# Optimization experiments

Measured on AMD Instinct MI355X. Metric: run time of the kernel, lower is better.

Reference implementation:

```python
import jax, jax.numpy as jnp
import numpy as np

N_NODES = 100000
N_EDGES = 1000000
N_INPUT = 64
N_HIDDEN = 64
K = 8


def setup_inputs() -> dict:
    key = jax.random.key(0)
    k1, k2, k3, k4 = jax.random.split(key, 4)
    x = jax.random.normal(k1, (N_NODES, N_INPUT), dtype=jnp.float32)
    edge_index = jax.random.randint(k2, (2, N_EDGES), 0, N_NODES, dtype=jnp.int64)
    # ChebConv has K independent [in, out] weight matrices (Glorot-ish scale) and a bias.
    weight = jax.random.normal(k3, (K, N_INPUT, N_HIDDEN), dtype=jnp.float32) * (1.0 / np.sqrt(N_INPUT))
    bias = jax.random.normal(k4, (N_HIDDEN,), dtype=jnp.float32) * 0.01
    return {"x": x, "edge_index": edge_index, "weight": weight, "bias": bias}


def _cheb_edge_norm(edge_index, num_nodes):
    # PyG ChebConv sym normalization with default lambda_max=2.0:
    #   L_hat = (2/lambda_max) * (I - D^-1/2 A D^-1/2) - I = -D^-1/2 A D^-1/2
    # (the diagonal +1 from the Laplacian and the -1 self-loop cancel exactly).
    src, dst = edge_index[0], edge_index[1]
    ones = jnp.ones(src.shape[0], dtype=jnp.float32)
    deg = jax.ops.segment_sum(ones, src, num_segments=num_nodes)
    deg_inv_sqrt = jnp.where(deg > 0, jax.lax.rsqrt(jnp.maximum(deg, 1.0)), 0.0)
    return -deg_inv_sqrt[src] * deg_inv_sqrt[dst]  # [E]


def reference(x, edge_index, weight, bias):
    num_nodes = x.shape[0]
    src, dst = edge_index[0], edge_index[1]
    norm = _cheb_edge_norm(edge_index, num_nodes)

    def prop(h):  # h: [N, F] -> L_hat @ h via gather-multiply-scatter over edges
        return jax.ops.segment_sum(norm[:, None] * h[src], dst, num_segments=num_nodes)

    # Chebyshev recursion: T0 = x, T1 = L_hat x, Tk = 2 L_hat T_{k-1} - T_{k-2}
    Tx0 = x
    out = Tx0 @ weight[0]
    Tx1 = prop(Tx0)
    out = out + Tx1 @ weight[1]
    for k in range(2, weight.shape[0]):
        Tx2 = 2.0 * prop(Tx1) - Tx0
        out = out + Tx2 @ weight[k]
        Tx0, Tx1 = Tx1, Tx2
    out = out + bias
    # bn=False path: ReLU then dropout (identity in eval mode)
    return jax.nn.relu(out)
```

## Files before the change

### kernel.cpp

```cpp
#include <hip/hip_runtime.h>
#include <hip/hip_bf16.h>

typedef __attribute__((ext_vector_type(8))) short s16x8;
typedef __attribute__((ext_vector_type(4))) float f32x4;

#define HC 48
#define RBH 6400
#define RBS 3200

static __device__ __forceinline__ unsigned short f2bf(float f) {
    unsigned int u = __float_as_uint(f);
    unsigned int r = (u + 0x7FFFu + ((u >> 16) & 1u)) >> 16;
    return (unsigned short)r;
}

__global__ __launch_bounds__(256) void k_hist(const int* __restrict__ eidx,
                                              unsigned short* __restrict__ partials,
                                              int N, int E, int HR) {
    __shared__ int h[RBH];
    int b = blockIdx.x;
    int job = b / (HR * HC);
    int rc = b % (HR * HC);
    int r = rc / HC, c = rc % HC;
    int lo = r * RBH;
    int nb = min(RBH, N - lo);
    if (nb <= 0) return;
    for (int i = threadIdx.x; i < nb; i += 256) h[i] = 0;
    __syncthreads();
    const int* vals = eidx + (size_t)job * E;
    int e0 = (int)(((long long)E * c / HC) & ~3LL);
    int e1 = (c == HC - 1) ? E : (int)(((long long)E * (c + 1) / HC) & ~3LL);
    int e = e0 + threadIdx.x * 4;
    for (; e + 4 <= e1; e += 1024) {
        int4 v = *reinterpret_cast<const int4*>(vals + e);
        unsigned r0 = (unsigned)(v.x - lo), r1 = (unsigned)(v.y - lo);
        unsigned r2 = (unsigned)(v.z - lo), r3 = (unsigned)(v.w - lo);
        if (r0 < (unsigned)nb) atomicAdd(&h[r0], 1);
        if (r1 < (unsigned)nb) atomicAdd(&h[r1], 1);
        if (r2 < (unsigned)nb) atomicAdd(&h[r2], 1);
        if (r3 < (unsigned)nb) atomicAdd(&h[r3], 1);
    }
    if (threadIdx.x == 0)
        for (int t = e1 & ~3; t < e1; ++t) {
            unsigned rel = (unsigned)(vals[t] - lo);
            if (rel < (unsigned)nb) atomicAdd(&h[rel], 1);
        }
    __syncthreads();
    unsigned short* outp = partials + ((size_t)(job * HC + c)) * N + lo;
    for (int i = threadIdx.x; i < nb; i += 256) outp[i] = (unsigned short)h[i];
}

__global__ void k_reduce(const unsigned short* __restrict__ partials,
                         float* __restrict__ dis, int* __restrict__ cnt, int N) {
    int n = blockIdx.x * blockDim.x + threadIdx.x;
    if (n >= N) return;
    int dsum = 0, csum = 0;
    for (int c = 0; c < HC; ++c) {
        dsum += partials[(size_t)c * N + n];
        csum += partials[(size_t)(HC + c) * N + n];
    }
    dis[n] = dsum > 0 ? rsqrtf((float)dsum) : 0.f;
    cnt[n] = csum;
}

__global__ void k_scan1(const int* __restrict__ cnt, int* __restrict__ incl,
                        int* __restrict__ bsum, int N) {
    __shared__ int sm[1024];
    int t = threadIdx.x;
    int i = blockIdx.x * 1024 + t;
    sm[t] = (i < N) ? cnt[i] : 0;
    __syncthreads();
    for (int off = 1; off < 1024; off <<= 1) {
        int add = (t >= off) ? sm[t - off] : 0;
        __syncthreads();
        sm[t] += add;
        __syncthreads();
    }
    if (i < N) incl[i] = sm[t];
    if (t == 1023) bsum[blockIdx.x] = sm[1023];
}

__global__ void k_scan2(const int* __restrict__ bsum, int* __restrict__ boff,
                        int nb, int* __restrict__ rowptr, int N) {
    if (threadIdx.x == 0 && blockIdx.x == 0) {
        int run = 0;
        for (int b = 0; b < nb; ++b) { boff[b] = run; run += bsum[b]; }
        rowptr[N] = run;
    }
}

__global__ void k_scan3(const int* __restrict__ cnt, const int* __restrict__ boff,
                        int* __restrict__ rowptr,
                        const unsigned short* __restrict__ pdst,
                        int* __restrict__ cbase, int N) {
    int i = blockIdx.x * 1024 + threadIdx.x;
    if (i >= N) return;
    int ex = rowptr[i] - cnt[i] + boff[blockIdx.x];
    rowptr[i] = ex;
    int run = ex;
    for (int c = 0; c < HC; ++c) {
        size_t idx = (size_t)c * N + i;
        cbase[idx] = run;
        run += pdst[idx];
    }
}

__global__ __launch_bounds__(256) void k_scatter(
        const int* __restrict__ src, const int* __restrict__ dst,
        const int* __restrict__ cbase, int* __restrict__ srcs, int N, int E) {
    __shared__ int cur[RBS];
    int r = blockIdx.x / HC, c = blockIdx.x % HC;
    int lo = r * RBS;
    int nb = min(RBS, N - lo);
    if (nb <= 0) return;
    for (int i = threadIdx.x; i < nb; i += 256)
        cur[i] = cbase[(size_t)c * N + lo + i];
    __syncthreads();
    int e0 = (int)(((long long)E * c / HC) & ~3LL);
    int e1 = (c == HC - 1) ? E : (int)(((long long)E * (c + 1) / HC) & ~3LL);
    int e = e0 + threadIdx.x * 4;
    for (; e + 4 <= e1; e += 1024) {
        int4 d4 = *reinterpret_cast<const int4*>(dst + e);
        unsigned r0 = (unsigned)(d4.x - lo), r1 = (unsigned)(d4.y - lo);
        unsigned r2 = (unsigned)(d4.z - lo), r3 = (unsigned)(d4.w - lo);
        if (r0 < (unsigned)nb) srcs[atomicAdd(&cur[r0], 1)] = src[e];
        if (r1 < (unsigned)nb) srcs[atomicAdd(&cur[r1], 1)] = src[e + 1];
        if (r2 < (unsigned)nb) srcs[atomicAdd(&cur[r2], 1)] = src[e + 2];
        if (r3 < (unsigned)nb) srcs[atomicAdd(&cur[r3], 1)] = src[e + 3];
    }
    if (threadIdx.x == 0)
        for (int t = e1 & ~3; t < e1; ++t) {
            unsigned rel = (unsigned)(dst[t] - lo);
            if (rel < (unsigned)nb) srcs[atomicAdd(&cur[rel], 1)] = src[t];
        }
}

__global__ void k_pack(const float* __restrict__ x, const float* __restrict__ dis,
                       const float* __restrict__ W,
                       unsigned short* __restrict__ tb0, unsigned short* __restrict__ ysA,
                       unsigned short* __restrict__ ysB, unsigned short* __restrict__ wt,
                       int N, int K) {
    int t = blockIdx.x * blockDim.x + threadIdx.x;
    int nys = (N + 1) * 32;
    if (t < nys) {
        int row = t >> 5, p = t & 31;
        size_t o = ((size_t)row << 6) + (p << 1);
        if (row == N) {
            *(unsigned*)(ysA + o) = 0;
            *(unsigned*)(ysB + o) = 0;
            return;
        }
        float2 v = *reinterpret_cast<const float2*>(x + o);
        float dv = dis[row];
        *(unsigned*)(tb0 + o) = (unsigned)f2bf(v.x) | ((unsigned)f2bf(v.y) << 16);
        *(unsigned*)(ysA + o) = (unsigned)f2bf(v.x * dv) | ((unsigned)f2bf(v.y * dv) << 16);
    } else {
        int u = t - nys;
        if (u < K * 4096) {
            float v = W[u];
            int k = u >> 12;
            int r = u & 4095;
            int i = r >> 6;
            int j = r & 63;
            wt[(size_t)j * (K * 64) + (k << 6) + i] = f2bf(v);
        }
    }
}

static __device__ __forceinline__ void addrow(float* acc, uint4 t) {
    acc[0] += __uint_as_float(t.x << 16);
    acc[1] += __uint_as_float(t.x & 0xffff0000u);
    acc[2] += __uint_as_float(t.y << 16);
    acc[3] += __uint_as_float(t.y & 0xffff0000u);
    acc[4] += __uint_as_float(t.z << 16);
    acc[5] += __uint_as_float(t.z & 0xffff0000u);
    acc[6] += __uint_as_float(t.w << 16);
    acc[7] += __uint_as_float(t.w & 0xffff0000u);
}

__global__ __launch_bounds__(256) void k_prop(
        const unsigned short* __restrict__ Ysin,
        const unsigned short* __restrict__ Tm2,
        unsigned short* __restrict__ Tout,
        unsigned short* __restrict__ Ysout,
        const int* __restrict__ rowptr, const int* __restrict__ srcs,
        const float* __restrict__ dis,
        int N, int E, float scale, float beta, int wys) {
    int gt = blockIdx.x * blockDim.x + threadIdx.x;
    int wave0 = (gt >> 6) << 3;
    int lane = gt & 63;
    int g = lane >> 3;
    int i = lane & 7;
    int node = wave0 + g;
    bool live = node < N;
    int rs = 0, deg = 0;
    if (live) {
        rs = rowptr[node];
        deg = rowptr[node + 1] - rs;
    }
    int wmax = deg;
#pragma unroll
    for (int m = 8; m <= 32; m <<= 1) {
        int o = __shfl_xor(wmax, m);
        wmax = o > wmax ? o : wmax;
    }
    float acc[8];
#pragma unroll
    for (int j = 0; j < 8; ++j) acc[j] = 0.f;
    for (int e = 0; e < wmax; e += 8) {
        int b = rs + e;
        int s[8];
#pragma unroll
        for (int q = 0; q < 8; ++q)
            s[q] = (e + q < deg) ? srcs[min(b + q, E - 1)] : N;
        uint4 t[8];
#pragma unroll
        for (int q = 0; q < 8; ++q)
            t[q] = *reinterpret_cast<const uint4*>(Ysin + ((size_t)s[q] << 6) + (i << 3));
#pragma unroll
        for (int q = 0; q < 8; ++q) addrow(acc, t[q]);
    }
    if (live) {
        float dv = dis[node];
        float sc = -scale * dv;
        size_t base = ((size_t)node << 6) + (i << 3);
        float r[8];
#pragma unroll
        for (int j = 0; j < 8; ++j) r[j] = sc * acc[j];
        if (beta != 0.f) {
            uint4 pv = *reinterpret_cast<const uint4*>(Tm2 + base);
            r[0] = fmaf(beta, __uint_as_float(pv.x << 16), r[0]);
            r[1] = fmaf(beta, __uint_as_float(pv.x & 0xffff0000u), r[1]);
            r[2] = fmaf(beta, __uint_as_float(pv.y << 16), r[2]);
            r[3] = fmaf(beta, __uint_as_float(pv.y & 0xffff0000u), r[3]);
            r[4] = fmaf(beta, __uint_as_float(pv.z << 16), r[4]);
            r[5] = fmaf(beta, __uint_as_float(pv.z & 0xffff0000u), r[5]);
            r[6] = fmaf(beta, __uint_as_float(pv.w << 16), r[6]);
            r[7] = fmaf(beta, __uint_as_float(pv.w & 0xffff0000u), r[7]);
        }
        uint4 ov;
        ov.x = (unsigned)f2bf(r[0]) | ((unsigned)f2bf(r[1]) << 16);
        ov.y = (unsigned)f2bf(r[2]) | ((unsigned)f2bf(r[3]) << 16);
        ov.z = (unsigned)f2bf(r[4]) | ((unsigned)f2bf(r[5]) << 16);
        ov.w = (unsigned)f2bf(r[6]) | ((unsigned)f2bf(r[7]) << 16);
        *reinterpret_cast<uint4*>(Tout + base) = ov;
        if (wys) {
            uint4 yv;
            yv.x = (unsigned)f2bf(r[0] * dv) | ((unsigned)f2bf(r[1] * dv) << 16);
            yv.y = (unsigned)f2bf(r[2] * dv) | ((unsigned)f2bf(r[3] * dv) << 16);
            yv.z = (unsigned)f2bf(r[4] * dv) | ((unsigned)f2bf(r[5] * dv) << 16);
            yv.w = (unsigned)f2bf(r[6] * dv) | ((unsigned)f2bf(r[7] * dv) << 16);
            *reinterpret_cast<uint4*>(Ysout + base) = yv;
        }
    }
}

template <int KS>
__global__ __launch_bounds__(256) void k_gemm(const unsigned short* __restrict__ tb,
                                              const unsigned short* __restrict__ wt,
                                              const float* __restrict__ bias,
                                              float* __restrict__ out,
                                              int N, int NF) {
    constexpr int NB = KS / 2;
    __shared__ unsigned short lds[KS * 512];
    int lane = threadIdx.x & 63;
    int w = threadIdx.x >> 6;
    int l16 = lane & 15;
    int quad = lane >> 4;
    const int KI = KS * 32;

    s16x8 afr[KS];
    {
        const unsigned short* wrow = wt + (size_t)(w * 16 + l16) * KI + quad * 8;
#pragma unroll
        for (int ks = 0; ks < KS; ++ks)
            afr[ks] = *reinterpret_cast<const s16x8*>(wrow + ks * 32);
    }
    f32x4 bias4 = *reinterpret_cast<const f32x4*>(bias + w * 16 + quad * 4);

    int ntiles = N >> 4;
    for (int t = blockIdx.x; t < ntiles; t += gridDim.x) {
        const char* tilebase = (const char*)tb + (size_t)t * 2048;
#pragma unroll
        for (int inst = 0; inst < 2 * NB; ++inst) {
            if ((inst & 3) != w) continue;
            int kbuf = inst >> 1;
            int j = inst & 1;
            int p = j * 64 + lane;
            int nrow = p >> 3;
            int s = (p & 7) ^ (nrow & 7);
            const char* g = tilebase + (size_t)kbuf * NF * 2 + nrow * 128 + s * 16;
            __builtin_amdgcn_global_load_lds(
                (const __attribute__((address_space(1))) unsigned int*)g,
                (__attribute__((address_space(3))) unsigned int*)(lds + inst * 512),
                16, 0, 0);
        }
        __syncthreads();
        f32x4 acc = {0.f, 0.f, 0.f, 0.f};
#pragma unroll
        for (int ks = 0; ks < KS; ++ks) {
            int kbuf = ks >> 1, half = ks & 1;
            int sph = (half * 4 + quad) ^ (l16 & 7);
            s16x8 bf = *reinterpret_cast<const s16x8*>(
                lds + kbuf * 1024 + l16 * 64 + sph * 8);
            acc = __builtin_amdgcn_mfma_f32_16x16x32_bf16(afr[ks], bf, acc, 0, 0, 0);
        }
        float* orow = out + (size_t)(t * 16 + l16) * 64 + w * 16 + quad * 4;
        f32x4 r;
#pragma unroll
        for (int q = 0; q < 4; ++q) {
            float v = acc[q] + bias4[q];
            r[q] = v > 0.f ? v : 0.f;
        }
        *reinterpret_cast<f32x4*>(orow) = r;
        __syncthreads();
    }
}

extern "C" void kernel_launch(void* const* d_in, const int* in_sizes, int n_in,
                              void* d_out, int out_size, void* d_ws, size_t ws_size,
                              hipStream_t stream) {
    const float* x    = (const float*)d_in[0];
    const int*   eidx = (const int*)d_in[1];
    const float* W    = (const float*)d_in[2];
    const float* bias = (const float*)d_in[3];
    float* out = (float*)d_out;

    const int NF = in_sizes[0];
    const int N  = NF / 64;
    const int E  = in_sizes[1] / 2;
    const int K  = in_sizes[2] / 4096;

    const int* src = eidx;
    const int* dst = eidx + E;

    char* ws = (char*)d_ws;
    size_t off = 0;
    auto alloc = [&](size_t bytes) -> char* {
        char* p = ws + off;
        off = (off + bytes + 255) & ~(size_t)255;
        return p;
    };
    unsigned short* Tb = (unsigned short*)alloc((size_t)K * NF * 2);
    unsigned short* Ys[2];
    Ys[0] = (unsigned short*)alloc((size_t)(N + 1) * 64 * 2);
    Ys[1] = (unsigned short*)alloc((size_t)(N + 1) * 64 * 2);
    unsigned short* Wt = (unsigned short*)alloc((size_t)64 * K * 64 * 2);
    int*   srcs   = (int*)alloc((size_t)E * 4);
    int*   rowptr = (int*)alloc((size_t)(N + 1) * 4);
    int*   cnt    = (int*)alloc((size_t)N * 4);
    unsigned short* partials = (unsigned short*)alloc((size_t)2 * HC * N * 2);
    int*   cbase  = (int*)alloc((size_t)HC * N * 4);
    float* dis  = (float*)alloc((size_t)N * 4);
    int*   bsum = (int*)alloc(1024);
    int*   boff = (int*)alloc(1024);
    (void)ws_size; (void)n_in; (void)out_size;

    int HR = (N + RBH - 1) / RBH;
    int SR = (N + RBS - 1) / RBS;
    const unsigned short* pdst = partials + (size_t)HC * N;

    k_hist<<<2 * HR * HC, 256, 0, stream>>>(eidx, partials, N, E, HR);
    k_reduce<<<(N + 255) / 256, 256, 0, stream>>>(partials, dis, cnt, N);
    int nb = (N + 1023) / 1024;
    k_scan1<<<nb, 1024, 0, stream>>>(cnt, rowptr, bsum, N);
    k_scan2<<<1, 64, 0, stream>>>(bsum, boff, nb, rowptr, N);
    k_scan3<<<nb, 1024, 0, stream>>>(cnt, boff, rowptr, pdst, cbase, N);
    k_scatter<<<SR * HC, 256, 0, stream>>>(src, dst, cbase, srcs, N, E);
    int packn = (N + 1) * 32 + K * 4096;
    k_pack<<<(packn + 255) / 256, 256, 0, stream>>>(x, dis, W, Tb, Ys[0], Ys[1], Wt, N, K);

    int waves = (N + 7) / 8;
    int pblocks = (waves * 64 + 255) / 256;
    for (int p = 1; p < K; ++p) {
        float scale = (p == 1) ? 1.f : 2.f;
        float beta  = (p == 1) ? 0.f : -1.f;
        const unsigned short* Tm2 = Tb + (size_t)(p >= 2 ? p - 2 : 0) * NF;
        k_prop<<<pblocks, 256, 0, stream>>>(
            Ys[(p - 1) & 1], Tm2, Tb + (size_t)p * NF, Ys[p & 1],
            rowptr, srcs, dis, N, E, scale, beta, p < K - 1 ? 1 : 0);
    }

    if (K == 8)      k_gemm<16><<<1024, 256, 0, stream>>>(Tb, Wt, bias, out, N, NF);
    else if (K == 4) k_gemm<8><<<1024, 256, 0, stream>>>(Tb, Wt, bias, out, N, NF);
    else if (K == 2) k_gemm<4><<<1024, 256, 0, stream>>>(Tb, Wt, bias, out, N, NF);
    else if (K == 1) k_gemm<2><<<1024, 256, 0, stream>>>(Tb, Wt, bias, out, N, NF);
}
```

Before: 342.7 us.

## Sort nodes by degree and carry per-edge source weights in propagation

Result: slower. 507.4 us (+48.1%).

```diff
diff --git a/kernel.cpp b/kernel.cpp
--- a/kernel.cpp
+++ b/kernel.cpp
@@ -7,6 +7,7 @@
 #define HC 48
 #define RBH 6400
 #define RBS 3200
+#define DB 64
 
 static __device__ __forceinline__ unsigned short f2bf(float f) {
     unsigned int u = __float_as_uint(f);
@@ -135,27 +136,79 @@
         }
 }
 
-__global__ void k_pack(const float* __restrict__ x, const float* __restrict__ dis,
-                       const float* __restrict__ W,
-                       unsigned short* __restrict__ tb0, unsigned short* __restrict__ ysA,
-                       unsigned short* __restrict__ ysB, unsigned short* __restrict__ wt,
-                       int N, int K) {
+__global__ __launch_bounds__(256) void k_dhist(const int* __restrict__ cnt,
+                                               int* __restrict__ dpart, int N) {
+    __shared__ int h[DB];
+    if (threadIdx.x < DB) h[threadIdx.x] = 0;
+    __syncthreads();
+    int i = blockIdx.x * 256 + threadIdx.x;
+    if (i < N) atomicAdd(&h[min(cnt[i], DB - 1)], 1);
+    __syncthreads();
+    if (threadIdx.x < DB) dpart[blockIdx.x * DB + threadIdx.x] = h[threadIdx.x];
+}
+
+__global__ void k_dscan(int* __restrict__ dpart, int nb2) {
+    __shared__ int tot[DB], base[DB];
+    int b = threadIdx.x;
+    int run = 0;
+    for (int blk = 0; blk < nb2; ++blk) {
+        int v = dpart[blk * DB + b];
+        dpart[blk * DB + b] = run;
+        run += v;
+    }
+    tot[b] = run;
+    __syncthreads();
+    if (b == 0) {
+        int r = 0;
+        for (int j = 0; j < DB; ++j) { base[j] = r; r += tot[j]; }
+    }
+    __syncthreads();
+    for (int blk = 0; blk < nb2; ++blk)
+        dpart[blk * DB + b] += base[b];
+}
+
+__global__ __launch_bounds__(256) void k_dscat(const int* __restrict__ cnt,
+                                               const int* __restrict__ rowptr,
+                                               const int* __restrict__ dpart,
+                                               int* __restrict__ perm,
+                                               int2* __restrict__ rdeg, int N) {
+    __shared__ int cur[DB];
+    if (threadIdx.x < DB) cur[threadIdx.x] = dpart[blockIdx.x * DB + threadIdx.x];
+    __syncthreads();
+    int i = blockIdx.x * 256 + threadIdx.x;
+    if (i < N) {
+        int d = cnt[i];
+        int pos = atomicAdd(&cur[min(d, DB - 1)], 1);
+        perm[pos] = i;
+        rdeg[pos] = make_int2(rowptr[i], d);
+    }
+}
+
+__global__ void k_pay(const int* __restrict__ srcs, const float* __restrict__ dis,
+                      int2* __restrict__ pay, int E) {
+    int e = blockIdx.x * blockDim.x + threadIdx.x;
+    if (e < E) {
+        int s = srcs[e];
+        pay[e] = make_int2(s, __float_as_int(dis[s]));
+    }
+}
+
+__global__ void k_pack(const float* __restrict__ x, const float* __restrict__ W,
+                       unsigned short* __restrict__ tb, unsigned short* __restrict__ wt,
+                       int N, int K, int NR) {
     int t = blockIdx.x * blockDim.x + threadIdx.x;
-    int nys = (N + 1) * 32;
-    if (t < nys) {
+    int nx = N * 32;
+    if (t < nx) {
         int row = t >> 5, p = t & 31;
         size_t o = ((size_t)row << 6) + (p << 1);
-        if (row == N) {
-            *(unsigned*)(ysA + o) = 0;
-            *(unsigned*)(ysB + o) = 0;
-            return;
-        }
         float2 v = *reinterpret_cast<const float2*>(x + o);
-        float dv = dis[row];
-        *(unsigned*)(tb0 + o) = (unsigned)f2bf(v.x) | ((unsigned)f2bf(v.y) << 16);
-        *(unsigned*)(ysA + o) = (unsigned)f2bf(v.x * dv) | ((unsigned)f2bf(v.y * dv) << 16);
+        *(unsigned*)(tb + o) = (unsigned)f2bf(v.x) | ((unsigned)f2bf(v.y) << 16);
+    } else if (t < nx + K * 32) {
+        int u = t - nx;
+        int lvl = u >> 5, p = u & 31;
+        *(unsigned*)(tb + (size_t)lvl * NR + ((size_t)N << 6) + (p << 1)) = 0;
     } else {
-        int u = t - nys;
+        int u = t - nx - K * 32;
         if (u < K * 4096) {
             float v = W[u];
             int k = u >> 12;
@@ -167,36 +220,37 @@
     }
 }
 
-static __device__ __forceinline__ void addrow(float* acc, uint4 t) {
-    acc[0] += __uint_as_float(t.x << 16);
-    acc[1] += __uint_as_float(t.x & 0xffff0000u);
-    acc[2] += __uint_as_float(t.y << 16);
-    acc[3] += __uint_as_float(t.y & 0xffff0000u);
-    acc[4] += __uint_as_float(t.z << 16);
-    acc[5] += __uint_as_float(t.z & 0xffff0000u);
-    acc[6] += __uint_as_float(t.w << 16);
-    acc[7] += __uint_as_float(t.w & 0xffff0000u);
+static __device__ __forceinline__ void addrow_w(float* acc, uint4 t, float w) {
+    acc[0] = fmaf(w, __uint_as_float(t.x << 16), acc[0]);
+    acc[1] = fmaf(w, __uint_as_float(t.x & 0xffff0000u), acc[1]);
+    acc[2] = fmaf(w, __uint_as_float(t.y << 16), acc[2]);
+    acc[3] = fmaf(w, __uint_as_float(t.y & 0xffff0000u), acc[3]);
+    acc[4] = fmaf(w, __uint_as_float(t.z << 16), acc[4]);
+    acc[5] = fmaf(w, __uint_as_float(t.z & 0xffff0000u), acc[5]);
+    acc[6] = fmaf(w, __uint_as_float(t.w << 16), acc[6]);
+    acc[7] = fmaf(w, __uint_as_float(t.w & 0xffff0000u), acc[7]);
 }
 
 __global__ __launch_bounds__(256) void k_prop(
-        const unsigned short* __restrict__ Ysin,
+        const unsigned short* __restrict__ Tin,
         const unsigned short* __restrict__ Tm2,
         unsigned short* __restrict__ Tout,
-        unsigned short* __restrict__ Ysout,
-        const int* __restrict__ rowptr, const int* __restrict__ srcs,
-        const float* __restrict__ dis,
-        int N, int E, float scale, float beta, int wys) {
+        const int2* __restrict__ rdeg, const int* __restrict__ perm,
+        const int2* __restrict__ pay, const float* __restrict__ dis,
+        int N, float scale, float beta) {
     int gt = blockIdx.x * blockDim.x + threadIdx.x;
-    int wave0 = (gt >> 6) << 3;
+    int slot0 = (gt >> 6) << 3;
     int lane = gt & 63;
     int g = lane >> 3;
     int i = lane & 7;
-    int node = wave0 + g;
-    bool live = node < N;
-    int rs = 0, deg = 0;
+    int slot = slot0 + g;
+    bool live = slot < N;
+    int node = 0, rs = 0, deg = 0;
     if (live) {
-        rs = rowptr[node];
-        deg = rowptr[node + 1] - rs;
+        int2 rd = rdeg[slot];
+        node = perm[slot];
+        rs = rd.x;
+        deg = rd.y;
     }
     int wmax = deg;
 #pragma unroll
@@ -208,17 +262,17 @@
 #pragma unroll
     for (int j = 0; j < 8; ++j) acc[j] = 0.f;
     for (int e = 0; e < wmax; e += 8) {
-        int b = rs + e;
-        int s[8];
+        int2 p[8];
 #pragma unroll
         for (int q = 0; q < 8; ++q)
-            s[q] = (e + q < deg) ? srcs[min(b + q, E - 1)] : N;
+            p[q] = (e + q < deg) ? pay[rs + e + q] : make_int2(N, 0);
         uint4 t[8];
 #pragma unroll
         for (int q = 0; q < 8; ++q)
-            t[q] = *reinterpret_cast<const uint4*>(Ysin + ((size_t)s[q] << 6) + (i << 3));
-#pragma unroll
-        for (int q = 0; q < 8; ++q) addrow(acc, t[q]);
+            t[q] = *reinterpret_cast<const uint4*>(Tin + ((size_t)p[q].x << 6) + (i << 3));
+#pragma unroll
+        for (int q = 0; q < 8; ++q)
+            addrow_w(acc, t[q], __int_as_float(p[q].y));
     }
     if (live) {
         float dv = dis[node];
@@ -244,14 +298,6 @@
         ov.z = (unsigned)f2bf(r[4]) | ((unsigned)f2bf(r[5]) << 16);
         ov.w = (unsigned)f2bf(r[6]) | ((unsigned)f2bf(r[7]) << 16);
         *reinterpret_cast<uint4*>(Tout + base) = ov;
-        if (wys) {
-            uint4 yv;
-            yv.x = (unsigned)f2bf(r[0] * dv) | ((unsigned)f2bf(r[1] * dv) << 16);
-            yv.y = (unsigned)f2bf(r[2] * dv) | ((unsigned)f2bf(r[3] * dv) << 16);
-            yv.z = (unsigned)f2bf(r[4] * dv) | ((unsigned)f2bf(r[5] * dv) << 16);
-            yv.w = (unsigned)f2bf(r[6] * dv) | ((unsigned)f2bf(r[7] * dv) << 16);
-            *reinterpret_cast<uint4*>(Ysout + base) = yv;
-        }
     }
 }
 
@@ -260,7 +306,7 @@
                                               const unsigned short* __restrict__ wt,
                                               const float* __restrict__ bias,
                                               float* __restrict__ out,
-                                              int N, int NF) {
+                                              int N, int NR) {
     constexpr int NB = KS / 2;
     __shared__ unsigned short lds[KS * 512];
     int lane = threadIdx.x & 63;
@@ -289,7 +335,7 @@
             int p = j * 64 + lane;
             int nrow = p >> 3;
             int s = (p & 7) ^ (nrow & 7);
-            const char* g = tilebase + (size_t)kbuf * NF * 2 + nrow * 128 + s * 16;
+            const char* g = tilebase + (size_t)kbuf * NR * 2 + nrow * 128 + s * 16;
             __builtin_amdgcn_global_load_lds(
                 (const __attribute__((address_space(1))) unsigned int*)g,
                 (__attribute__((address_space(3))) unsigned int*)(lds + inst * 512),
@@ -330,6 +376,7 @@
     const int N  = NF / 64;
     const int E  = in_sizes[1] / 2;
     const int K  = in_sizes[2] / 4096;
+    const int NR = (N + 1) * 64;
 
     const int* src = eidx;
     const int* dst = eidx + E;
@@ -341,17 +388,19 @@
         off = (off + bytes + 255) & ~(size_t)255;
         return p;
     };
-    unsigned short* Tb = (unsigned short*)alloc((size_t)K * NF * 2);
-    unsigned short* Ys[2];
-    Ys[0] = (unsigned short*)alloc((size_t)(N + 1) * 64 * 2);
-    Ys[1] = (unsigned short*)alloc((size_t)(N + 1) * 64 * 2);
+    unsigned short* Tb = (unsigned short*)alloc((size_t)K * NR * 2);
     unsigned short* Wt = (unsigned short*)alloc((size_t)64 * K * 64 * 2);
     int*   srcs   = (int*)alloc((size_t)E * 4);
+    int2*  pay    = (int2*)alloc((size_t)E * 8);
     int*   rowptr = (int*)alloc((size_t)(N + 1) * 4);
     int*   cnt    = (int*)alloc((size_t)N * 4);
     unsigned short* partials = (unsigned short*)alloc((size_t)2 * HC * N * 2);
     int*   cbase  = (int*)alloc((size_t)HC * N * 4);
     float* dis  = (float*)alloc((size_t)N * 4);
+    int*   perm = (int*)alloc((size_t)N * 4);
+    int2*  rdeg = (int2*)alloc((size_t)N * 8);
+    int nb2 = (N + 255) / 256;
+    int*   dpart = (int*)alloc((size_t)nb2 * DB * 4);
     int*   bsum = (int*)alloc(1024);
     int*   boff = (int*)alloc(1024);
     (void)ws_size; (void)n_in; (void)out_size;
@@ -367,22 +416,26 @@
     k_scan2<<<1, 64, 0, stream>>>(bsum, boff, nb, rowptr, N);
     k_scan3<<<nb, 1024, 0, stream>>>(cnt, boff, rowptr, pdst, cbase, N);
     k_scatter<<<SR * HC, 256, 0, stream>>>(src, dst, cbase, srcs, N, E);
-    int packn = (N + 1) * 32 + K * 4096;
-    k_pack<<<(packn + 255) / 256, 256, 0, stream>>>(x, dis, W, Tb, Ys[0], Ys[1], Wt, N, K);
+    k_dhist<<<nb2, 256, 0, stream>>>(cnt, dpart, N);
+    k_dscan<<<1, DB, 0, stream>>>(dpart, nb2);
+    k_dscat<<<nb2, 256, 0, stream>>>(cnt, rowptr, dpart, perm, rdeg, N);
+    k_pay<<<(E + 255) / 256, 256, 0, stream>>>(srcs, dis, pay, E);
+    int packn = N * 32 + K * 32 + K * 4096;
+    k_pack<<<(packn + 255) / 256, 256, 0, stream>>>(x, W, Tb, Wt, N, K, NR);
 
     int waves = (N + 7) / 8;
     int pblocks = (waves * 64 + 255) / 256;
     for (int p = 1; p < K; ++p) {
         float scale = (p == 1) ? 1.f : 2.f;
         float beta  = (p == 1) ? 0.f : -1.f;
-        const unsigned short* Tm2 = Tb + (size_t)(p >= 2 ? p - 2 : 0) * NF;
+        const unsigned short* Tin = Tb + (size_t)(p - 1) * NR;
+        const unsigned short* Tm2 = Tb + (size_t)(p >= 2 ? p - 2 : 0) * NR;
         k_prop<<<pblocks, 256, 0, stream>>>(
-            Ys[(p - 1) & 1], Tm2, Tb + (size_t)p * NF, Ys[p & 1],
-            rowptr, srcs, dis, N, E, scale, beta, p < K - 1 ? 1 : 0);
-    }
-
-    if (K == 8)      k_gemm<16><<<1024, 256, 0, stream>>>(Tb, Wt, bias, out, N, NF);
-    else if (K == 4) k_gemm<8><<<1024, 256, 0, stream>>>(Tb, Wt, bias, out, N, NF);
-    else if (K == 2) k_gemm<4><<<1024, 256, 0, stream>>>(Tb, Wt, bias, out, N, NF);
-    else if (K == 1) k_gemm<2><<<1024, 256, 0, stream>>>(Tb, Wt, bias, out, N, NF);
-}
+            Tin, Tm2, Tb + (size_t)p * NR, rdeg, perm, pay, dis, N, scale, beta);
+    }
+
+    if (K == 8)      k_gemm<16><<<1024, 256, 0, stream>>>(Tb, Wt, bias, out, N, NR);
+    else if (K == 4) k_gemm<8><<<1024, 256, 0, stream>>>(Tb, Wt, bias, out, N, NR);
+    else if (K == 2) k_gemm<4><<<1024, 256, 0, stream>>>(Tb, Wt, bias, out, N, NR);
+    else if (K == 1) k_gemm<2><<<1024, 256, 0, stream>>>(Tb, Wt, bias, out, N, NR);
+}
```
